# Optimization experiments

Hardware: AMD Instinct MI355X
Metric: run time of the kernel (lower is better)

The kernel has to match this reference:

```python
import jax, jax.numpy as jnp
import numpy as np

N = 100000
IN_C = 128
HID_C = 128
OUT_C = 128
E = 3200000


def setup_inputs() -> dict:
    key = jax.random.key(0)
    ks = jax.random.split(key, 8)
    x = jax.random.normal(ks[0], (N, IN_C), dtype=jnp.float32)
    edge_index = jax.random.randint(ks[1], (2, E), 0, N, dtype=jnp.int64)
    edge_weight = jnp.ones((E,), dtype=jnp.float32)
    s = 1.0 / np.sqrt(HID_C)
    W_conv = jax.random.uniform(ks[2], (HID_C, IN_C), jnp.float32, -s, s)
    b_conv = jnp.zeros((HID_C,), dtype=jnp.float32)
    W_fc = jax.random.uniform(ks[3], (HID_C, HID_C), jnp.float32, -s, s)
    b_fc = jax.random.uniform(ks[4], (HID_C,), jnp.float32, -s, s)
    W_fc2 = jax.random.uniform(ks[5], (OUT_C, HID_C), jnp.float32, -s, s)
    b_fc2 = jax.random.uniform(ks[6], (OUT_C,), jnp.float32, -s, s)
    return {"x": x, "edge_index": edge_index, "edge_weight": edge_weight,
            "W_conv": W_conv, "b_conv": b_conv, "W_fc": W_fc, "b_fc": b_fc,
            "W_fc2": W_fc2, "b_fc2": b_fc2}


def _gcn_conv(x, edge_index, edge_weight, W_conv, b_conv):
    n = x.shape[0]
    # add self-loops with weight 1 (PyG GCNConv default)
    loop = jnp.arange(n, dtype=edge_index.dtype)
    src = jnp.concatenate([edge_index[0], loop])
    dst = jnp.concatenate([edge_index[1], loop])
    ew = jnp.concatenate([edge_weight, jnp.ones((n,), dtype=edge_weight.dtype)])
    # symmetric normalization: deg^-1/2[src] * w * deg^-1/2[dst]
    deg = jax.ops.segment_sum(ew, dst, num_segments=n)
    dinv = jnp.where(deg > 0, jax.lax.rsqrt(jnp.where(deg > 0, deg, 1.0)), 0.0)
    norm = dinv[src] * ew * dinv[dst]  # [E+N]
    h = x @ W_conv.T                   # [N, hid], bias-free linear first
    msg = h[src] * norm[:, None]       # gather + scale
    agg = jax.ops.segment_sum(msg, dst, num_segments=n)  # scatter-add
    return agg + b_conv


def reference(x, edge_index, edge_weight, W_conv, b_conv, W_fc, b_fc, W_fc2, b_fc2):
    h = _gcn_conv(x, edge_index, edge_weight, W_conv, b_conv)
    h = jax.nn.relu(h)
    h = jax.nn.relu(h @ W_fc.T + b_fc)
    return h @ W_fc2.T + b_fc2
```

## Files before the change

kernel.cpp:

```cpp
#include <hip/hip_runtime.h>

typedef short bf16x8 __attribute__((ext_vector_type(8)));
typedef short bf16x4 __attribute__((ext_vector_type(4)));
typedef float f32x4 __attribute__((ext_vector_type(4)));
typedef float f32x2 __attribute__((ext_vector_type(2)));

#define PS 32
#define CAPP 1312
#define NB 256
#define CAPB 17536

__device__ __forceinline__ unsigned short f2bf(float f) {
    unsigned int u = __float_as_uint(f);
    u = (u + 0x7FFFu + ((u >> 16) & 1u)) >> 16;
    return (unsigned short)u;
}

__global__ __launch_bounds__(1024) void scatA_k(const int* __restrict__ ei,
                                                const float* __restrict__ ew,
                                                int* __restrict__ bucketCnt,
                                                int2* __restrict__ bstage,
                                                const float* __restrict__ Wc,
                                                const float* __restrict__ Wf,
                                                const float* __restrict__ W2,
                                                unsigned short* __restrict__ wcb,
                                                unsigned short* __restrict__ wfb,
                                                unsigned short* __restrict__ w2b,
                                                int E, int NBK, int EPB) {
    __shared__ int cntl[256];
    __shared__ int basel[256];
    const int b = blockIdx.x, tid = threadIdx.x;

    if (b < 12) {
        int t = (b << 10) | tid;
        int a = t >> 12, idx = t & 4095;
        const float4* s4 = (const float4*)(a == 0 ? Wc : (a == 1 ? Wf : W2));
        unsigned short* dw = (a == 0 ? wcb : (a == 1 ? wfb : w2b));
        float4 v = s4[idx];
        ushort4 o;
        o.x = f2bf(v.x); o.y = f2bf(v.y); o.z = f2bf(v.z); o.w = f2bf(v.w);
        *(ushort4*)(dw + idx * 4) = o;
    }

    if (tid < 256) cntl[tid] = 0;
    __syncthreads();
    const int s = b * EPB, e = min(E, s + EPB);
    for (int i = s + tid; i < e; i += 1024)
        atomicAdd(&cntl[ei[E + i] >> 9], 1);
    __syncthreads();
    if (tid < NBK) {
        int c = cntl[tid];
        basel[tid] = tid * CAPB + (c ? atomicAdd(&bucketCnt[tid], c) : 0);
        cntl[tid] = 0;
    }
    __syncthreads();
    for (int i = s + tid; i < e; i += 1024) {
        int src = ei[i];
        int dst = ei[E + i];
        float w = ew[i];
        int bk = dst >> 9;
        int lidx = atomicAdd(&cntl[bk], 1);
        int pos = basel[bk] + lidx;
        if (pos < (bk + 1) * CAPB)
            bstage[pos] = make_int2(src | ((dst & 31) << 17) | (((dst >> 5) & 15) << 22),
                                    __float_as_int(w));
    }
}

__global__ __launch_bounds__(1024) void scatB_k(const int* __restrict__ bucketCnt,
                                                const int2* __restrict__ bstage,
                                                int* __restrict__ partCnt,
                                                int2* __restrict__ regions,
                                                int P) {
    __shared__ int cl[16];
    __shared__ int cur[16];
    const int bk = blockIdx.x, tid = threadIdx.x;
    const int cnt = min(bucketCnt[bk], CAPB);
    const int2* bs = bstage + (size_t)bk * CAPB;

    if (tid < 16) cl[tid] = 0;
    __syncthreads();
    for (int i = tid; i < cnt; i += 1024)
        atomicAdd(&cl[((unsigned)bs[i].x >> 22) & 15], 1);
    __syncthreads();
    if (tid < 16) {
        int p = bk * 16 + tid;
        if (p < P) partCnt[p] = cl[tid];
        cur[tid] = 0;
    }
    __syncthreads();
    for (int i = tid; i < cnt; i += 1024) {
        int2 r = bs[i];
        unsigned x = (unsigned)r.x;
        int pl = (x >> 22) & 15;
        int pos = atomicAdd(&cur[pl], 1);
        if (pos < CAPP) {
            int p = bk * 16 + pl;
            regions[(size_t)p * CAPP + pos] =
                make_int2((int)(x & 0x1FFFFu) | (int)(((x >> 17) & 31u) << 24), r.y);
        }
    }
}

__global__ __launch_bounds__(256) void dgemm1_k(const float* __restrict__ x,
                                                const unsigned short* __restrict__ Wcb,
                                                const int* __restrict__ partCnt,
                                                const int2* __restrict__ regions,
                                                float* __restrict__ dinv,
                                                int* __restrict__ nodeOff,
                                                unsigned short* __restrict__ h,
                                                int M, int P) {
    __shared__ __align__(16) unsigned short Wl[128 * 136];
    __shared__ float degl[64];
    __shared__ int cl[64];
    __shared__ float dl64[64];
    const int tid = threadIdx.x;
    if (tid < 64) { degl[tid] = 0.f; cl[tid] = 0; }

#pragma unroll
    for (int i = 0; i < 8; ++i) {
        int c = i * 256 + tid;
        int r = c >> 4, col = (c & 15) * 8;
        *(bf16x8*)&Wl[r * 136 + col] = *(const bf16x8*)(Wcb + c * 8);
    }
    __syncthreads();

#pragma unroll
    for (int q = 0; q < 2; ++q) {
        int p = blockIdx.x * 2 + q;
        if (p < P) {
            const int cnt = min(partCnt[p], CAPP);
            const int2* reg = regions + (size_t)p * CAPP;
            for (int i = tid; i < cnt; i += 256) {
                int2 r = reg[i];
                int dl = q * 32 + ((r.x >> 24) & 31);
                atomicAdd(&cl[dl], 1);
                atomicAdd(&degl[dl], __int_as_float(r.y));
            }
        }
    }
    __syncthreads();
    if (tid < 64) {
        int cn = cl[tid];
        int v = cn;
#pragma unroll
        for (int off = 1; off < 32; off <<= 1) {
            int u = __shfl_up(v, off, 32);
            if ((tid & 31) >= off) v += u;
        }
        int node = blockIdx.x * 64 + tid;
        float d = rsqrtf(1.0f + degl[tid]);
        if (node < M) { nodeOff[node] = v - cn; dinv[node] = d; }
        dl64[tid] = d;
    }
    __syncthreads();

    const int wave = tid >> 6, lane = tid & 63;
    const int m = lane & 15, quad = lane >> 4;
    const int rowBase = blockIdx.x * 64 + wave * 16;
    int arow = rowBase + m;
    int arowc = arow < M ? arow : (M - 1);

    bf16x8 afrag[4];
    const float* pa = x + (size_t)arowc * 128 + quad * 8;
#pragma unroll
    for (int kc = 0; kc < 4; ++kc) {
        float4 v0 = *(const float4*)(pa + kc * 32);
        float4 v1 = *(const float4*)(pa + kc * 32 + 4);
        bf16x8 f;
        f[0] = (short)f2bf(v0.x); f[1] = (short)f2bf(v0.y);
        f[2] = (short)f2bf(v0.z); f[3] = (short)f2bf(v0.w);
        f[4] = (short)f2bf(v1.x); f[5] = (short)f2bf(v1.y);
        f[6] = (short)f2bf(v1.z); f[7] = (short)f2bf(v1.w);
        afrag[kc] = f;
    }

    float dv[4];
#pragma unroll
    for (int r = 0; r < 4; ++r)
        dv[r] = dl64[wave * 16 + quad * 4 + r];

#pragma unroll
    for (int nt = 0; nt < 8; ++nt) {
        f32x4 acc = {0.f, 0.f, 0.f, 0.f};
        const unsigned short* wb = &Wl[(nt * 16 + m) * 136 + quad * 8];
#pragma unroll
        for (int kc = 0; kc < 4; ++kc) {
            bf16x8 bfrag = *(const bf16x8*)(wb + kc * 32);
            acc = __builtin_amdgcn_mfma_f32_16x16x32_bf16(afrag[kc], bfrag, acc, 0, 0, 0);
        }
        const int col = nt * 16 + m;
#pragma unroll
        for (int r = 0; r < 4; ++r) {
            int row = rowBase + quad * 4 + r;
            if (row < M)
                h[((size_t)(col >> 6) * M + row) * 64 + (col & 63)] = f2bf(acc[r] * dv[r]);
        }
    }
}

__global__ __launch_bounds__(256) void aggF_k(const int* __restrict__ partCnt,
                                              const int* __restrict__ nodeOff,
                                              const int2* __restrict__ regions,
                                              const unsigned short* __restrict__ h,
                                              const float* __restrict__ dinv,
                                              const float* __restrict__ bconv,
                                              unsigned short* __restrict__ h2, int N) {
    __shared__ __align__(16) int2 stag[CAPP];
    __shared__ int cstart[PS + 1];
    __shared__ int wcur[PS];
    const int p = blockIdx.x, tid = threadIdx.x;
    const int cnt = min(partCnt[p], CAPP);
    const int2* reg = regions + (size_t)p * CAPP;

    if (tid < PS) {
        int node = p * PS + tid;
        int o = (node < N) ? nodeOff[node] : cnt;
        cstart[tid] = o;
        wcur[tid] = o;
    } else if (tid == PS) {
        cstart[PS] = cnt;
    }
    __syncthreads();
    for (int i = tid; i < cnt; i += 256) {
        int2 r = reg[i];
        int pos = atomicAdd(&wcur[(r.x >> 24) & 31], 1);
        stag[pos] = make_int2((r.x & 0xFFFFFF) << 7, r.y);
    }
    __syncthreads();

    const int wave = tid >> 6, lane = tid & 63;
    const int g = lane >> 4;
    const int c4 = (lane & 15) * 4;
    const int c4b = c4 * 2;

#define ACC2(q, w) {                                                        \
        unsigned ux = (unsigned)(q).x, uy = (unsigned)(q).y;                \
        f32x2 ww; ww[0] = (w); ww[1] = (w);                                 \
        f32x2 v01, v23;                                                     \
        v01[0] = __uint_as_float(ux << 16);                                 \
        v01[1] = __uint_as_float(ux & 0xFFFF0000u);                         \
        v23[0] = __uint_as_float(uy << 16);                                 \
        v23[1] = __uint_as_float(uy & 0xFFFF0000u);                         \
        a01 = v01 * ww + a01; a23 = v23 * ww + a23; }

#pragma unroll
    for (int hh = 0; hh < 2; ++hh) {
        const char* hb = (const char*)h + ((size_t)hh * (size_t)N << 7);
        for (int nl = wave; nl < PS; nl += 4) {
            int n = p * PS + nl;
            if (n >= N) continue;
            const int s = cstart[nl], e = cstart[nl + 1];
            f32x2 a01 = {0.f, 0.f}, a23 = {0.f, 0.f};
            int j = s;
            const int e32 = s + ((e - s) & ~31);
            for (; j < e32; j += 32) {
                int2 r0 = stag[j + g];
                int2 r1 = stag[j + 4 + g];
                int2 r2 = stag[j + 8 + g];
                int2 r3 = stag[j + 12 + g];
                int2 r4 = stag[j + 16 + g];
                int2 r5 = stag[j + 20 + g];
                int2 r6 = stag[j + 24 + g];
                int2 r7 = stag[j + 28 + g];
                int2 q0 = *(const int2*)(hb + ((unsigned)r0.x + c4b));
                int2 q1 = *(const int2*)(hb + ((unsigned)r1.x + c4b));
                int2 q2 = *(const int2*)(hb + ((unsigned)r2.x + c4b));
                int2 q3 = *(const int2*)(hb + ((unsigned)r3.x + c4b));
                int2 q4 = *(const int2*)(hb + ((unsigned)r4.x + c4b));
                int2 q5 = *(const int2*)(hb + ((unsigned)r5.x + c4b));
                int2 q6 = *(const int2*)(hb + ((unsigned)r6.x + c4b));
                int2 q7 = *(const int2*)(hb + ((unsigned)r7.x + c4b));
                ACC2(q0, __int_as_float(r0.y));
                ACC2(q1, __int_as_float(r1.y));
                ACC2(q2, __int_as_float(r2.y));
                ACC2(q3, __int_as_float(r3.y));
                ACC2(q4, __int_as_float(r4.y));
                ACC2(q5, __int_as_float(r5.y));
                ACC2(q6, __int_as_float(r6.y));
                ACC2(q7, __int_as_float(r7.y));
            }
            const int e16 = s + ((e - s) & ~15);
            for (; j < e16; j += 16) {
                int2 r0 = stag[j + g];
                int2 r1 = stag[j + 4 + g];
                int2 r2 = stag[j + 8 + g];
                int2 r3 = stag[j + 12 + g];
                int2 q0 = *(const int2*)(hb + ((unsigned)r0.x + c4b));
                int2 q1 = *(const int2*)(hb + ((unsigned)r1.x + c4b));
                int2 q2 = *(const int2*)(hb + ((unsigned)r2.x + c4b));
                int2 q3 = *(const int2*)(hb + ((unsigned)r3.x + c4b));
                ACC2(q0, __int_as_float(r0.y));
                ACC2(q1, __int_as_float(r1.y));
                ACC2(q2, __int_as_float(r2.y));
                ACC2(q3, __int_as_float(r3.y));
            }
            for (; j < e; j += 8) {
                int j0 = j + g, j1 = j + 4 + g;
                int2 r0 = stag[j0 < e ? j0 : s];
                int2 r1 = stag[j1 < e ? j1 : s];
                float w0 = (j0 < e) ? __int_as_float(r0.y) : 0.f;
                float w1 = (j1 < e) ? __int_as_float(r1.y) : 0.f;
                int2 q0 = *(const int2*)(hb + ((unsigned)r0.x + c4b));
                int2 q1 = *(const int2*)(hb + ((unsigned)r1.x + c4b));
                ACC2(q0, w0);
                ACC2(q1, w1);
            }
            float acc[4] = {a01[0], a01[1], a23[0], a23[1]};
#pragma unroll
            for (int k = 0; k < 4; ++k) {
                float v = acc[k];
                v += __shfl_xor(v, 16, 64);
                v += __shfl_xor(v, 32, 64);
                acc[k] = v;
            }
            if (g == 0) {
                float di = dinv[n];
                int2 qs = *(const int2*)(hb + (((size_t)(unsigned)n << 7) + c4b));
                float4 b = *(const float4*)(bconv + hh * 64 + c4);
                unsigned ux = (unsigned)qs.x, uy = (unsigned)qs.y;
                bf16x4 o;
                o[0] = (short)f2bf(fmaxf(di * (acc[0] + __uint_as_float(ux << 16)) + b.x, 0.f));
                o[1] = (short)f2bf(fmaxf(di * (acc[1] + __uint_as_float(ux & 0xFFFF0000u)) + b.y, 0.f));
                o[2] = (short)f2bf(fmaxf(di * (acc[2] + __uint_as_float(uy << 16)) + b.z, 0.f));
                o[3] = (short)f2bf(fmaxf(di * (acc[3] + __uint_as_float(uy & 0xFFFF0000u)) + b.w, 0.f));
                *(bf16x4*)(h2 + (size_t)n * 128 + hh * 64 + c4) = o;
            }
        }
    }
#undef ACC2
}

__global__ __launch_bounds__(256) void gemm23_k(const unsigned short* __restrict__ h2,
                                                const unsigned short* __restrict__ Wfb,
                                                const float* __restrict__ bfc,
                                                const unsigned short* __restrict__ W2b,
                                                const float* __restrict__ b2,
                                                float* __restrict__ out, int M) {
    __shared__ __align__(16) unsigned short Wl[128 * 136];
    __shared__ __align__(16) unsigned short Tl[64 * 136];
    const int tid = threadIdx.x;

#pragma unroll
    for (int i = 0; i < 8; ++i) {
        int c = i * 256 + tid;
        int r = c >> 4, col = (c & 15) * 8;
        *(bf16x8*)&Wl[r * 136 + col] = *(const bf16x8*)(Wfb + c * 8);
    }
    __syncthreads();

    const int wave = tid >> 6, lane = tid & 63;
    const int m = lane & 15, quad = lane >> 4;
    const int rowBase = blockIdx.x * 64 + wave * 16;
    int arow = rowBase + m;
    int arowc = arow < M ? arow : (M - 1);

    bf16x8 afrag[4];
    {
        const unsigned short* pa = h2 + (size_t)arowc * 128 + quad * 8;
#pragma unroll
        for (int kc = 0; kc < 4; ++kc)
            afrag[kc] = *(const bf16x8*)(pa + kc * 32);
    }

#pragma unroll
    for (int nt = 0; nt < 8; ++nt) {
        f32x4 acc = {0.f, 0.f, 0.f, 0.f};
        const unsigned short* wb = &Wl[(nt * 16 + m) * 136 + quad * 8];
#pragma unroll
        for (int kc = 0; kc < 4; ++kc) {
            bf16x8 bfrag = *(const bf16x8*)(wb + kc * 32);
            acc = __builtin_amdgcn_mfma_f32_16x16x32_bf16(afrag[kc], bfrag, acc, 0, 0, 0);
        }
        const int col = nt * 16 + m;
        float bv = bfc[col];
#pragma unroll
        for (int r = 0; r < 4; ++r) {
            int rowl = wave * 16 + quad * 4 + r;
            Tl[rowl * 136 + col] = f2bf(fmaxf(acc[r] + bv, 0.f));
        }
    }
    __syncthreads();

#pragma unroll
    for (int i = 0; i < 8; ++i) {
        int c = i * 256 + tid;
        int r = c >> 4, col = (c & 15) * 8;
        *(bf16x8*)&Wl[r * 136 + col] = *(const bf16x8*)(W2b + c * 8);
    }
    __syncthreads();

    bf16x8 afrag2[4];
    {
        const unsigned short* pa = &Tl[(wave * 16 + m) * 136 + quad * 8];
#pragma unroll
        for (int kc = 0; kc < 4; ++kc)
            afrag2[kc] = *(const bf16x8*)(pa + kc * 32);
    }
#pragma unroll
    for (int nt = 0; nt < 8; ++nt) {
        f32x4 acc = {0.f, 0.f, 0.f, 0.f};
        const unsigned short* wb = &Wl[(nt * 16 + m) * 136 + quad * 8];
#pragma unroll
        for (int kc = 0; kc < 4; ++kc) {
            bf16x8 bfrag = *(const bf16x8*)(wb + kc * 32);
            acc = __builtin_amdgcn_mfma_f32_16x16x32_bf16(afrag2[kc], bfrag, acc, 0, 0, 0);
        }
        const int col = nt * 16 + m;
        float bv = b2[col];
#pragma unroll
        for (int r = 0; r < 4; ++r) {
            int row = rowBase + quad * 4 + r;
            if (row < M)
                out[(size_t)row * 128 + col] = acc[r] + bv;
        }
    }
}

extern "C" void kernel_launch(void* const* d_in, const int* in_sizes, int n_in,
                              void* d_out, int out_size, void* d_ws, size_t ws_size,
                              hipStream_t stream) {
    const float* x  = (const float*)d_in[0];
    const int* ei   = (const int*)d_in[1];
    const float* ew = (const float*)d_in[2];
    const float* Wc = (const float*)d_in[3];
    const float* bc = (const float*)d_in[4];
    const float* Wf = (const float*)d_in[5];
    const float* bf = (const float*)d_in[6];
    const float* W2 = (const float*)d_in[7];
    const float* b2 = (const float*)d_in[8];
    float* out = (float*)d_out;

    const int N = in_sizes[0] / 128;
    const int E = in_sizes[2];
    const int P = (N + PS - 1) / PS;
    const int NBK = (N + 511) >> 9;

    auto align256 = [](size_t v) { return (v + 255) & ~(size_t)255; };
    char* ws = (char*)d_ws;
    size_t off = 0;
    float* dinv  = (float*)(ws + off); off += align256((size_t)N * 4);
    int* nodeOff = (int*)(ws + off);   off += align256((size_t)N * 4);
    int* partCnt = (int*)(ws + off);   off += align256((size_t)P * 4);
    int* bucketCnt = (int*)(ws + off); off += align256((size_t)NBK * 4);
    unsigned short* wcb = (unsigned short*)(ws + off); off += align256(16384 * 2);
    unsigned short* wfb = (unsigned short*)(ws + off); off += align256(16384 * 2);
    unsigned short* w2b = (unsigned short*)(ws + off); off += align256(16384 * 2);
    unsigned short* h  = (unsigned short*)(ws + off); off += (size_t)N * 256;
    unsigned short* h2 = (unsigned short*)(ws + off);

    int2* bstage = (int2*)h;

    int2* regions = (int2*)out;

    const int EPB = (E + NB - 1) / NB;

    hipMemsetAsync(bucketCnt, 0, (size_t)NBK * 4, stream);
    scatA_k<<<NB, 1024, 0, stream>>>(ei, ew, bucketCnt, bstage, Wc, Wf, W2, wcb, wfb, w2b, E, NBK, EPB);
    scatB_k<<<NBK, 1024, 0, stream>>>(bucketCnt, bstage, partCnt, regions, P);
    dgemm1_k<<<(N + 63) / 64, 256, 0, stream>>>(x, wcb, partCnt, regions, dinv, nodeOff, h, N, P);
    aggF_k<<<P, 256, 0, stream>>>(partCnt, nodeOff, regions, h, dinv, bc, h2, N);
    gemm23_k<<<(N + 63) / 64, 256, 0, stream>>>(h2, wfb, bf, w2b, b2, out, N);
}
```

Before: 337.5 us.

## Sort edges by destination node in bucket pass, drop per-partition re-sort

The second scatter pass now histograms edges per destination node instead of per partition. It computes degrees, dinv and per-node offsets there and writes edges already grouped by node into the partition regions. This removes the degree/offset re-read of regions from the first GEMM kernel and the shared-memory counting sort from the aggregation kernel, which now copies regions straight into LDS. The cost is more shared atomics per edge (count, float degree and cursor) on 512 bins in the scatter kernel.

```diff
diff --git a/kernel.cpp b/kernel.cpp
--- a/kernel.cpp
+++ b/kernel.cpp
@@ -62,96 +62,83 @@
         int lidx = atomicAdd(&cntl[bk], 1);
         int pos = basel[bk] + lidx;
         if (pos < (bk + 1) * CAPB)
-            bstage[pos] = make_int2(src | ((dst & 31) << 17) | (((dst >> 5) & 15) << 22),
-                                    __float_as_int(w));
+            bstage[pos] = make_int2(src | ((dst & 511) << 17), __float_as_int(w));
     }
 }
 
 __global__ __launch_bounds__(1024) void scatB_k(const int* __restrict__ bucketCnt,
                                                 const int2* __restrict__ bstage,
                                                 int* __restrict__ partCnt,
+                                                int* __restrict__ nodeOff,
+                                                float* __restrict__ dinv,
                                                 int2* __restrict__ regions,
-                                                int P) {
-    __shared__ int cl[16];
-    __shared__ int cur[16];
+                                                int P, int N) {
+    __shared__ int cnode[512];
+    __shared__ float degf[512];
     const int bk = blockIdx.x, tid = threadIdx.x;
     const int cnt = min(bucketCnt[bk], CAPB);
     const int2* bs = bstage + (size_t)bk * CAPB;
 
-    if (tid < 16) cl[tid] = 0;
-    __syncthreads();
-    for (int i = tid; i < cnt; i += 1024)
-        atomicAdd(&cl[((unsigned)bs[i].x >> 22) & 15], 1);
-    __syncthreads();
-    if (tid < 16) {
-        int p = bk * 16 + tid;
-        if (p < P) partCnt[p] = cl[tid];
-        cur[tid] = 0;
+    if (tid < 512) { cnode[tid] = 0; degf[tid] = 0.f; }
+    __syncthreads();
+    for (int i = tid; i < cnt; i += 1024) {
+        int2 r = bs[i];
+        int nl = ((unsigned)r.x >> 17) & 511;
+        atomicAdd(&cnode[nl], 1);
+        atomicAdd(&degf[nl], __int_as_float(r.y));
+    }
+    __syncthreads();
+    if (tid < 512) {
+        int cn = cnode[tid];
+        int v = cn;
+#pragma unroll
+        for (int off = 1; off < 32; off <<= 1) {
+            int u = __shfl_up(v, off, 32);
+            if ((tid & 31) >= off) v += u;
+        }
+        int n = bk * 512 + tid;
+        if (n < N) {
+            nodeOff[n] = v - cn;
+            dinv[n] = rsqrtf(1.0f + degf[tid]);
+        }
+        if ((tid & 31) == 31) {
+            int p = bk * 16 + (tid >> 5);
+            if (p < P) partCnt[p] = v;
+        }
+        cnode[tid] = v - cn;
     }
     __syncthreads();
     for (int i = tid; i < cnt; i += 1024) {
         int2 r = bs[i];
         unsigned x = (unsigned)r.x;
-        int pl = (x >> 22) & 15;
-        int pos = atomicAdd(&cur[pl], 1);
+        int nl = (x >> 17) & 511;
+        int pos = atomicAdd(&cnode[nl], 1);
         if (pos < CAPP) {
-            int p = bk * 16 + pl;
-            regions[(size_t)p * CAPP + pos] =
-                make_int2((int)(x & 0x1FFFFu) | (int)(((x >> 17) & 31u) << 24), r.y);
+            int p = bk * 16 + (nl >> 5);
+            regions[(size_t)p * CAPP + pos] = make_int2((int)((x & 0x1FFFFu) << 7), r.y);
         }
     }
 }
 
 __global__ __launch_bounds__(256) void dgemm1_k(const float* __restrict__ x,
                                                 const unsigned short* __restrict__ Wcb,
-                                                const int* __restrict__ partCnt,
-                                                const int2* __restrict__ regions,
-                                                float* __restrict__ dinv,
-                                                int* __restrict__ nodeOff,
+                                                const float* __restrict__ dinv,
                                                 unsigned short* __restrict__ h,
-                                                int M, int P) {
+                                                int M) {
     __shared__ __align__(16) unsigned short Wl[128 * 136];
-    __shared__ float degl[64];
-    __shared__ int cl[64];
     __shared__ float dl64[64];
     const int tid = threadIdx.x;
-    if (tid < 64) { degl[tid] = 0.f; cl[tid] = 0; }
+
+    if (tid < 64) {
+        int node = blockIdx.x * 64 + tid;
+        dl64[tid] = (node < M) ? dinv[node] : 0.f;
+    }
 
 #pragma unroll
     for (int i = 0; i < 8; ++i) {
         int c = i * 256 + tid;
         int r = c >> 4, col = (c & 15) * 8;
         *(bf16x8*)&Wl[r * 136 + col] = *(const bf16x8*)(Wcb + c * 8);
-    }
-    __syncthreads();
-
-#pragma unroll
-    for (int q = 0; q < 2; ++q) {
-        int p = blockIdx.x * 2 + q;
-        if (p < P) {
-            const int cnt = min(partCnt[p], CAPP);
-            const int2* reg = regions + (size_t)p * CAPP;
-            for (int i = tid; i < cnt; i += 256) {
-                int2 r = reg[i];
-                int dl = q * 32 + ((r.x >> 24) & 31);
-                atomicAdd(&cl[dl], 1);
-                atomicAdd(&degl[dl], __int_as_float(r.y));
-            }
-        }
-    }
-    __syncthreads();
-    if (tid < 64) {
-        int cn = cl[tid];
-        int v = cn;
-#pragma unroll
-        for (int off = 1; off < 32; off <<= 1) {
-            int u = __shfl_up(v, off, 32);
-            if ((tid & 31) >= off) v += u;
-        }
-        int node = blockIdx.x * 64 + tid;
-        float d = rsqrtf(1.0f + degl[tid]);
-        if (node < M) { nodeOff[node] = v - cn; dinv[node] = d; }
-        dl64[tid] = d;
     }
     __syncthreads();
 
@@ -208,25 +195,17 @@
                                               unsigned short* __restrict__ h2, int N) {
     __shared__ __align__(16) int2 stag[CAPP];
     __shared__ int cstart[PS + 1];
-    __shared__ int wcur[PS];
     const int p = blockIdx.x, tid = threadIdx.x;
     const int cnt = min(partCnt[p], CAPP);
     const int2* reg = regions + (size_t)p * CAPP;
 
     if (tid < PS) {
         int node = p * PS + tid;
-        int o = (node < N) ? nodeOff[node] : cnt;
-        cstart[tid] = o;
-        wcur[tid] = o;
+        cstart[tid] = (node < N) ? nodeOff[node] : cnt;
     } else if (tid == PS) {
         cstart[PS] = cnt;
     }
-    __syncthreads();
-    for (int i = tid; i < cnt; i += 256) {
-        int2 r = reg[i];
-        int pos = atomicAdd(&wcur[(r.x >> 24) & 31], 1);
-        stag[pos] = make_int2((r.x & 0xFFFFFF) << 7, r.y);
-    }
+    for (int i = tid; i < cnt; i += 256) stag[i] = reg[i];
     __syncthreads();
 
     const int wave = tid >> 6, lane = tid & 63;
@@ -457,8 +436,8 @@
 
     hipMemsetAsync(bucketCnt, 0, (size_t)NBK * 4, stream);
     scatA_k<<<NB, 1024, 0, stream>>>(ei, ew, bucketCnt, bstage, Wc, Wf, W2, wcb, wfb, w2b, E, NBK, EPB);
-    scatB_k<<<NBK, 1024, 0, stream>>>(bucketCnt, bstage, partCnt, regions, P);
-    dgemm1_k<<<(N + 63) / 64, 256, 0, stream>>>(x, wcb, partCnt, regions, dinv, nodeOff, h, N, P);
+    scatB_k<<<NBK, 1024, 0, stream>>>(bucketCnt, bstage, partCnt, nodeOff, dinv, regions, P, N);
+    dgemm1_k<<<(N + 63) / 64, 256, 0, stream>>>(x, wcb, dinv, h, N);
     aggF_k<<<P, 256, 0, stream>>>(partCnt, nodeOff, regions, h, dinv, bc, h2, N);
     gemm23_k<<<(N + 63) / 64, 256, 0, stream>>>(h2, wfb, bf, w2b, b2, out, N);
 }
```

Result: slower. 353.1 us (+4.6%).
